# Optimization experiments

Hardware: AMD Instinct MI355X
Metric: run time of the kernel (lower is better)

Reference implementation:

```python
import jax, jax.numpy as jnp
import numpy as np

B, H, S, D = 2, 16, 2048, 64

def setup_inputs() -> dict:
    key = jax.random.key(0)
    kq, kk, kv, km = jax.random.split(key, 4)
    Q = jax.random.normal(kq, (B, H, S, D), dtype=jnp.float32)
    K = jax.random.normal(kk, (B, H, S, D), dtype=jnp.float32)
    V = jax.random.normal(kv, (B, H, S, D), dtype=jnp.float32)
    attn_mask = jax.random.bernoulli(km, 0.5, (B, H, S, S))  # True = masked
    return {"Q": Q, "K": K, "V": V, "attn_mask": attn_mask}

def reference(Q, K, V, attn_mask):
    eps = 1e-12
    d_tensor = K.shape[-1]
    # scores: [B, H, S, S]
    scores = jnp.einsum('bhqd,bhkd->bhqk', Q, K) / np.sqrt(d_tensor).astype(jnp.float32)
    # Faithful to source: first fill mask==0 positions with -eps, then mask==True with -1e9.
    scores = jnp.where(attn_mask == 0, jnp.float32(-eps), scores)
    scores = jnp.where(attn_mask, jnp.float32(-1e9), scores)
    attn = jax.nn.softmax(scores, axis=-1)
    context = jnp.einsum('bhqk,bhkd->bhqd', attn, V)
    # dropout=0.0 (eval) -> identity
    return (context, attn)
```

## Files before the change

### kernel.cpp

```cpp
#include <hip/hip_runtime.h>
#include <hip/hip_bf16.h>
#include <stdint.h>

#define S 2048
#define D 64
#define BH 32
#define NROWS (BH * S)
#define CTX_ELEMS (NROWS * D)

typedef __attribute__((ext_vector_type(8))) __bf16 bf16x8;
typedef __attribute__((ext_vector_type(4))) float f32x4;

__global__ __launch_bounds__(256) void k_mask(const int* __restrict__ mask,
                                              float* __restrict__ attn,
                                              uint32_t* packed) {
    const int r = blockIdx.x;
    const int t = threadIdx.x;
    const long base = (long)r * S + t * 8;

    const int4 m0 = *(const int4*)(mask + base);
    const int4 m1 = *(const int4*)(mask + base + 4);
    int v[8] = {m0.x, m0.y, m0.z, m0.w, m1.x, m1.y, m1.z, m1.w};

    unsigned byte = 0;
    int cnt = 0;
#pragma unroll
    for (int j = 0; j < 8; ++j) {
        unsigned u = (v[j] == 0) ? 1u : 0u;
        byte |= u << j;
        cnt += (int)u;
    }

#pragma unroll
    for (int off = 32; off > 0; off >>= 1) cnt += __shfl_down(cnt, off, 64);

    __shared__ int wsum[4];
    __shared__ unsigned char bts[256];
    bts[t] = (unsigned char)byte;
    if ((t & 63) == 0) wsum[t >> 6] = cnt;
    __syncthreads();

    const int total = wsum[0] + wsum[1] + wsum[2] + wsum[3];
    const float inv = (total > 0) ? (1.0f / (float)total) : 0.0f;

    float4 a0, a1;
    a0.x = (byte & 1u)   ? inv : 0.0f;
    a0.y = (byte & 2u)   ? inv : 0.0f;
    a0.z = (byte & 4u)   ? inv : 0.0f;
    a0.w = (byte & 8u)   ? inv : 0.0f;
    a1.x = (byte & 16u)  ? inv : 0.0f;
    a1.y = (byte & 32u)  ? inv : 0.0f;
    a1.z = (byte & 64u)  ? inv : 0.0f;
    a1.w = (byte & 128u) ? inv : 0.0f;
    *(float4*)(attn + base)     = a0;
    *(float4*)(attn + base + 4) = a1;

    if (t < 64) {
        uint32_t w = (uint32_t)bts[4 * t]
                   | ((uint32_t)bts[4 * t + 1] << 8)
                   | ((uint32_t)bts[4 * t + 2] << 16)
                   | ((uint32_t)bts[4 * t + 3] << 24);
        packed[(long)r * 64 + t] = w;
    }
}

#define BM 128
__global__ __launch_bounds__(256) void k_ctx(const uint32_t* packed,
                                             const float* __restrict__ V,
                                             float* ctx) {
    const int qt = blockIdx.x;
    const int bh = blockIdx.y;
    const int t = threadIdx.x;
    const int lane = t & 63;
    const int w = t >> 6;
    const int l15 = lane & 15;
    const int lk = lane >> 4;
    const long rowbase = (long)bh * S + qt * BM;

    __shared__ uint32_t pk[BM][65];
    __shared__ float invs[BM];
    __shared__ __align__(16) __bf16 Vs[64][40];

    for (int i = t; i < BM * 64; i += 256) {
        pk[i >> 6][i & 63] = packed[(rowbase + (i >> 6)) * 64 + (i & 63)];
    }
    __syncthreads();

    if (t < BM) {
        int c = 0;
#pragma unroll
        for (int i = 0; i < 64; ++i) c += __popc(pk[t][i]);
        invs[t] = (c > 0) ? (1.0f / (float)c) : 0.0f;
    }

    f32x4 acc[2][4];
#pragma unroll
    for (int a = 0; a < 2; ++a)
#pragma unroll
        for (int b = 0; b < 4; ++b) acc[a][b] = f32x4{0.f, 0.f, 0.f, 0.f};

    const int vcol = t & 63;
    const int vkb = (t >> 6) * 8;

    for (int kk = 0; kk < S / 32; ++kk) {
        __syncthreads();
        {
            const float* vp = V + ((long)bh * S + kk * 32 + vkb) * 64 + vcol;
            bf16x8 vv;
#pragma unroll
            for (int j = 0; j < 8; ++j) vv[j] = (__bf16)vp[j * 64];
            *reinterpret_cast<bf16x8*>(&Vs[vcol][vkb]) = vv;
        }
        __syncthreads();

        bf16x8 afrag[2];
#pragma unroll
        for (int mt = 0; mt < 2; ++mt) {
            const uint32_t dw = pk[w * 32 + mt * 16 + l15][kk];
            const unsigned bby = (dw >> (lk * 8)) & 0xFFu;
            union { uint32_t u[4]; bf16x8 v; } au;
#pragma unroll
            for (int p = 0; p < 4; ++p) {
                uint32_t lo = ((bby >> (2 * p)) & 1u) ? 0x3F80u : 0u;
                uint32_t hi = ((bby >> (2 * p + 1)) & 1u) ? 0x3F800000u : 0u;
                au.u[p] = lo | hi;
            }
            afrag[mt] = au.v;
        }

#pragma unroll
        for (int nt = 0; nt < 4; ++nt) {
            bf16x8 bfrag = *reinterpret_cast<const bf16x8*>(&Vs[nt * 16 + l15][lk * 8]);
            acc[0][nt] = __builtin_amdgcn_mfma_f32_16x16x32_bf16(afrag[0], bfrag, acc[0][nt], 0, 0, 0);
            acc[1][nt] = __builtin_amdgcn_mfma_f32_16x16x32_bf16(afrag[1], bfrag, acc[1][nt], 0, 0, 0);
        }
    }

#pragma unroll
    for (int mt = 0; mt < 2; ++mt) {
#pragma unroll
        for (int ri = 0; ri < 4; ++ri) {
            const int rloc = w * 32 + mt * 16 + lk * 4 + ri;
            const float iv = invs[rloc];
            const long orow = rowbase + rloc;
#pragma unroll
            for (int nt = 0; nt < 4; ++nt) {
                ctx[orow * 64 + nt * 16 + l15] = acc[mt][nt][ri] * iv;
            }
        }
    }
}

extern "C" void kernel_launch(void* const* d_in, const int* in_sizes, int n_in,
                              void* d_out, int out_size, void* d_ws, size_t ws_size,
                              hipStream_t stream) {
    (void)in_sizes; (void)n_in; (void)d_ws; (void)ws_size; (void)out_size;
    const float* V = (const float*)d_in[2];
    const int* mask = (const int*)d_in[3];
    float* ctx = (float*)d_out;
    float* attn = (float*)d_out + (size_t)CTX_ELEMS;
    uint32_t* packed = (uint32_t*)d_out;

    k_mask<<<NROWS, 256, 0, stream>>>(mask, attn, packed);
    k_ctx<<<dim3(S / BM, BH), 256, 0, stream>>>(packed, V, ctx);
}
```

Before: 256.1 us.

## Load V fragments directly into registers with double buffering, drop LDS staging

```diff
diff --git a/kernel.cpp b/kernel.cpp
--- a/kernel.cpp
+++ b/kernel.cpp
@@ -30,7 +30,6 @@
         byte |= u << j;
         cnt += (int)u;
     }
-
 #pragma unroll
     for (int off = 32; off > 0; off >>= 1) cnt += __shfl_down(cnt, off, 64);
 
@@ -64,34 +63,43 @@
     }
 }
 
-#define BM 128
-__global__ __launch_bounds__(256) void k_ctx(const uint32_t* packed,
+#define BMC 128
+__global__ __launch_bounds__(256) void k_ctx(const uint32_t* __restrict__ packed,
                                              const float* __restrict__ V,
-                                             float* ctx) {
-    const int qt = blockIdx.x;
-    const int bh = blockIdx.y;
+                                             float* __restrict__ ctx) {
+    const int flat = blockIdx.y * (S / BMC) + blockIdx.x;
+    const int wid = (flat & 7) * 64 + (flat >> 3);
+    const int qt = wid & 15;
+    const int bh = wid >> 4;
+
     const int t = threadIdx.x;
     const int lane = t & 63;
     const int w = t >> 6;
     const int l15 = lane & 15;
     const int lk = lane >> 4;
-    const long rowbase = (long)bh * S + qt * BM;
 
-    __shared__ uint32_t pk[BM][65];
-    __shared__ float invs[BM];
-    __shared__ __align__(16) __bf16 Vs[64][40];
+    __shared__ uint32_t pkw[BMC * 65];
+    __shared__ float invs[BMC];
 
-    for (int i = t; i < BM * 64; i += 256) {
-        pk[i >> 6][i & 63] = packed[(rowbase + (i >> 6)) * 64 + (i & 63)];
+    const long R0 = (long)bh * S + qt * BMC;
+
+    for (int i = t; i < BMC * 64; i += 256) {
+        pkw[(i >> 6) * 65 + (i & 63)] = packed[(R0 + (i >> 6)) * 64 + (i & 63)];
     }
     __syncthreads();
 
-    if (t < BM) {
+    if (t < BMC) {
         int c = 0;
 #pragma unroll
-        for (int i = 0; i < 64; ++i) c += __popc(pk[t][i]);
+        for (int i = 0; i < 64; ++i) c += __popc(pkw[t * 65 + i]);
         invs[t] = (c > 0) ? (1.0f / (float)c) : 0.0f;
     }
+    __syncthreads();
+
+    const uint8_t* pkb = (const uint8_t*)pkw;
+    const uint8_t* aptr0 = pkb + (w * 32 + l15) * 260;
+    const uint8_t* aptr1 = pkb + (w * 32 + 16 + l15) * 260;
+    const float* vb = V + (long)bh * S * D + (long)lk * 8 * D + l15;
 
     f32x4 acc[2][4];
 #pragma unroll
@@ -99,41 +107,49 @@
 #pragma unroll
         for (int b = 0; b < 4; ++b) acc[a][b] = f32x4{0.f, 0.f, 0.f, 0.f};
 
-    const int vcol = t & 63;
-    const int vkb = (t >> 6) * 8;
+    float cur[32], nxt[32];
 
-    for (int kk = 0; kk < S / 32; ++kk) {
-        __syncthreads();
-        {
-            const float* vp = V + ((long)bh * S + kk * 32 + vkb) * 64 + vcol;
-            bf16x8 vv;
+    auto LOADB = [&](float* dst, int kk) {
+        const float* vp = vb + (long)kk * 32 * D;
 #pragma unroll
-            for (int j = 0; j < 8; ++j) vv[j] = (__bf16)vp[j * 64];
-            *reinterpret_cast<bf16x8*>(&Vs[vcol][vkb]) = vv;
+        for (int n4 = 0; n4 < 4; ++n4)
+#pragma unroll
+            for (int j = 0; j < 8; ++j)
+                dst[n4 * 8 + j] = vp[j * D + n4 * 16];
+    };
+
+    auto COMPUTE = [&](const float* buf, int kk) {
+        bf16x8 bf[4];
+#pragma unroll
+        for (int n4 = 0; n4 < 4; ++n4) {
+            bf16x8 x;
+#pragma unroll
+            for (int j = 0; j < 8; ++j) x[j] = (__bf16)buf[n4 * 8 + j];
+            bf[n4] = x;
         }
-        __syncthreads();
+        const uint32_t by0 = aptr0[kk * 4 + lk];
+        const uint32_t by1 = aptr1[kk * 4 + lk];
+        union { uint32_t u[4]; bf16x8 v; } a0, a1;
+#pragma unroll
+        for (int p = 0; p < 4; ++p) {
+            a0.u[p] = (((by0 >> (2 * p)) & 1u) ? 0x3F80u : 0u)
+                    | (((by0 >> (2 * p + 1)) & 1u) ? 0x3F800000u : 0u);
+            a1.u[p] = (((by1 >> (2 * p)) & 1u) ? 0x3F80u : 0u)
+                    | (((by1 >> (2 * p + 1)) & 1u) ? 0x3F800000u : 0u);
+        }
+#pragma unroll
+        for (int n4 = 0; n4 < 4; ++n4) {
+            acc[0][n4] = __builtin_amdgcn_mfma_f32_16x16x32_bf16(a0.v, bf[n4], acc[0][n4], 0, 0, 0);
+            acc[1][n4] = __builtin_amdgcn_mfma_f32_16x16x32_bf16(a1.v, bf[n4], acc[1][n4], 0, 0, 0);
+        }
+    };
 
-        bf16x8 afrag[2];
-#pragma unroll
-        for (int mt = 0; mt < 2; ++mt) {
-            const uint32_t dw = pk[w * 32 + mt * 16 + l15][kk];
-            const unsigned bby = (dw >> (lk * 8)) & 0xFFu;
-            union { uint32_t u[4]; bf16x8 v; } au;
-#pragma unroll
-            for (int p = 0; p < 4; ++p) {
-                uint32_t lo = ((bby >> (2 * p)) & 1u) ? 0x3F80u : 0u;
-                uint32_t hi = ((bby >> (2 * p + 1)) & 1u) ? 0x3F800000u : 0u;
-                au.u[p] = lo | hi;
-            }
-            afrag[mt] = au.v;
-        }
-
-#pragma unroll
-        for (int nt = 0; nt < 4; ++nt) {
-            bf16x8 bfrag = *reinterpret_cast<const bf16x8*>(&Vs[nt * 16 + l15][lk * 8]);
-            acc[0][nt] = __builtin_amdgcn_mfma_f32_16x16x32_bf16(afrag[0], bfrag, acc[0][nt], 0, 0, 0);
-            acc[1][nt] = __builtin_amdgcn_mfma_f32_16x16x32_bf16(afrag[1], bfrag, acc[1][nt], 0, 0, 0);
-        }
+    LOADB(cur, 0);
+    for (int kk = 0; kk < S / 32; kk += 2) {
+        LOADB(nxt, kk + 1);
+        COMPUTE(cur, kk);
+        if (kk + 2 < S / 32) LOADB(cur, kk + 2);
+        COMPUTE(nxt, kk + 1);
     }
 
 #pragma unroll
@@ -142,10 +158,10 @@
         for (int ri = 0; ri < 4; ++ri) {
             const int rloc = w * 32 + mt * 16 + lk * 4 + ri;
             const float iv = invs[rloc];
-            const long orow = rowbase + rloc;
+            const long orow = R0 + rloc;
 #pragma unroll
-            for (int nt = 0; nt < 4; ++nt) {
-                ctx[orow * 64 + nt * 16 + l15] = acc[mt][nt][ri] * iv;
+            for (int n4 = 0; n4 < 4; ++n4) {
+                ctx[orow * D + n4 * 16 + l15] = acc[mt][n4][ri] * iv;
             }
         }
     }
@@ -162,5 +178,5 @@
     uint32_t* packed = (uint32_t*)d_out;
 
     k_mask<<<NROWS, 256, 0, stream>>>(mask, attn, packed);
-    k_ctx<<<dim3(S / BM, BH), 256, 0, stream>>>(packed, V, ctx);
+    k_ctx<<<dim3(S / BMC, BH), 256, 0, stream>>>(packed, V, ctx);
 }
```

New measurement: 244.8 us. -4.4%, faster.
